# Kernel tuning notes

Measured on AMD Instinct MI355X. Metric: run time of the kernel, lower is better.

## Reference

```python
import jax, jax.numpy as jnp
import numpy as np

POLY_P = 3
POLY_N = 3
ACTIVATE = True
NUM_ATOMS = 100
BATCH = 100
N_TOTAL = NUM_ATOMS * BATCH          # 10000 nodes
N_EDGES = 1_000_000
F_COEF = 1.0
NCL = 3 * (POLY_P - 1) + 4 * (POLY_N - 1) + 8 + 4 + (12 if ACTIVATE else 0)  # 38
NFL = POLY_P + POLY_N + 3 + (3 if ACTIVATE else 0)                           # 12


def _safe_inv(v, eps=1e-2):
    # guard divide-by-near-zero in the negative-power library terms
    s = jnp.where(v >= 0, 1.0, -1.0)
    return 1.0 / jnp.where(jnp.abs(v) < eps, s * eps, v)


def coupled_fun_lib(x_i, x_j):
    # x_i, x_j: [E, 1] scalar node states gathered per edge
    d = x_j - x_i
    s = x_j + x_i
    feats = []
    for p in range(1, POLY_P):                      # 3*(P-1)
        feats += [x_i ** p, x_j ** p, d ** p]
    for n in range(1, POLY_N):                      # 4*(Q-1)
        feats += [_safe_inv(x_i) ** n, _safe_inv(x_j) ** n,
                  _safe_inv(d) ** n, _safe_inv(s) ** n]
    feats += [jnp.sin(d), jnp.cos(d), jnp.sin(s), jnp.cos(s),   # 8 trig
              jnp.sin(x_i), jnp.cos(x_i), jnp.sin(x_j), jnp.cos(x_j)]
    feats += [x_i * x_j, x_i * jnp.sin(x_j),                    # 4 cross terms
              x_j * jnp.sin(x_i), jnp.sin(d) * jnp.cos(s)]
    if ACTIVATE:                                    # 12 activation terms
        for v in (x_i, x_j, d, s):
            feats += [jnp.tanh(v), jax.nn.sigmoid(v), jax.nn.relu(v)]
    return jnp.concatenate(feats, axis=1)  # [E, NCL]


def fun_lib(x):
    # x: [N, 1]
    feats = [jnp.ones_like(x), jnp.sin(x), jnp.cos(x), x * jnp.sin(x)]
    for p in range(1, POLY_P):
        feats.append(x ** p)
    for n in range(1, POLY_N + 1):
        feats.append(_safe_inv(x) ** n)
    if ACTIVATE:
        feats += [jnp.tanh(x), jax.nn.sigmoid(x), jax.nn.relu(x)]
    return jnp.concatenate(feats, axis=1)  # [N, NFL]


def setup_inputs() -> dict:
    key = jax.random.key(0)
    k1, k2, k3 = jax.random.split(key, 3)
    x = jax.random.normal(k1, (N_TOTAL, 1), dtype=jnp.float32)
    edge_index = jax.random.randint(k2, (2, N_EDGES), 0, N_TOTAL, dtype=jnp.int32).astype(jnp.int64)
    c_mask = jnp.ones((NCL, 1), dtype=jnp.float32)
    f_mask = jnp.ones((NFL, 1), dtype=jnp.float32)
    wc_2 = jnp.concatenate([0.99 * jnp.ones((NCL, 1)), 0.01 * jnp.ones((NCL, 1))], 0).astype(jnp.float32)
    wf_2 = jnp.concatenate([0.99 * jnp.ones((NFL, 1)), 0.01 * jnp.ones((NFL, 1))], 0).astype(jnp.float32)
    edge_attr_all = jax.random.normal(k3, (NUM_ATOMS, NUM_ATOMS), dtype=jnp.float32)
    return {"t": 0, "x": x, "edge_index": edge_index, "c_mask": c_mask,
            "f_mask": f_mask, "wc_2": wc_2, "wf_2": wf_2,
            "edge_attr_all": edge_attr_all}


def reference(t, x, edge_index, c_mask, f_mask, wc_2, wf_2, edge_attr_all):
    src = edge_index[0]   # x_j (source)
    dst = edge_index[1]   # x_i (target / aggregation index)
    x_j = x[src]          # [E, 1]
    x_i = x[dst]          # [E, 1]

    # GSI_C: edge feature library (no_grad in torch -> stop_gradient)
    C_msg = jax.lax.stop_gradient(coupled_fun_lib(x_i, x_j))
    C_msg = jnp.concatenate([C_msg, -C_msg], axis=1)            # [E, 2*NCL]
    wc_1 = jnp.concatenate([c_mask, c_mask], axis=0)            # [2*NCL, 1]
    edge_attr = edge_attr_all[src % NUM_ATOMS, dst % NUM_ATOMS][:, None]  # [E, 1]
    msg = edge_attr * (C_msg @ (wc_1 * wc_2))                   # [E, 1]
    C = jax.ops.segment_sum(msg, dst, num_segments=N_TOTAL)     # 'add' aggr

    # GSI_F: node feature library
    F_msg = jax.lax.stop_gradient(fun_lib(x))
    F_msg = jnp.concatenate([F_msg, -F_msg], axis=1)            # [N, 2*NFL]
    wf_1 = jnp.concatenate([f_mask, f_mask], axis=0)
    F = F_msg @ (wf_1 * wf_2)                                   # [N, 1]

    return C + F_COEF * F
```

## Files before the change

kernel.cpp:

```cpp
#include <hip/hip_runtime.h>


#define NCL 38
#define NFL 12
#define NMAX 10240
#define EAN  10000
#define GRP 8

__device__ __forceinline__ float frcp(float v) { return __builtin_amdgcn_rcpf(v); }

__device__ __forceinline__ float safe_inv(float v) {
    float den = (fabsf(v) < 0.01f) ? ((v >= 0.0f) ? 0.01f : -0.01f) : v;
    return frcp(den);
}

__device__ __forceinline__ float edge_msg(float xi, float xj, const float* w) {
    float d = xj - xi;
    float s = xj + xi;
    float acc;
    acc  = w[0] * xi + w[1] * xj + w[2] * d;
    acc += w[3] * (xi * xi) + w[4] * (xj * xj) + w[5] * (d * d);
    float ii = safe_inv(xi), ij = safe_inv(xj), id = safe_inv(d), is = safe_inv(s);
    acc += w[6] * ii + w[7] * ij + w[8] * id + w[9] * is;
    acc += w[10] * (ii * ii) + w[11] * (ij * ij) + w[12] * (id * id) + w[13] * (is * is);
    float sd = __sinf(d), cd = __cosf(d);
    float ss = __sinf(s), cs = __cosf(s);
    float si = __sinf(xi), ci = __cosf(xi);
    float sj = __sinf(xj), cj = __cosf(xj);
    acc += w[14] * sd + w[15] * cd + w[16] * ss + w[17] * cs;
    acc += w[18] * si + w[19] * ci + w[20] * sj + w[21] * cj;
    acc += w[22] * (xi * xj) + w[23] * (xi * sj) + w[24] * (xj * si) + w[25] * (sd * cs);
    {
        float e = __expf(xi), e2 = e * e;
        acc += w[26] * ((e2 - 1.f) * frcp(e2 + 1.f)) + w[27] * (e * frcp(e + 1.f)) + w[28] * fmaxf(xi, 0.f);
    }
    {
        float e = __expf(xj), e2 = e * e;
        acc += w[29] * ((e2 - 1.f) * frcp(e2 + 1.f)) + w[30] * (e * frcp(e + 1.f)) + w[31] * fmaxf(xj, 0.f);
    }
    {
        float e = __expf(d), e2 = e * e;
        acc += w[32] * ((e2 - 1.f) * frcp(e2 + 1.f)) + w[33] * (e * frcp(e + 1.f)) + w[34] * fmaxf(d, 0.f);
    }
    {
        float e = __expf(s), e2 = e * e;
        acc += w[35] * ((e2 - 1.f) * frcp(e2 + 1.f)) + w[36] * (e * frcp(e + 1.f)) + w[37] * fmaxf(s, 0.f);
    }
    return acc;
}

__device__ __forceinline__ float node_F(float v, const float* wf) {
    float sv = __sinf(v), cv = __cosf(v);
    float iv = safe_inv(v);
    float e  = __expf(v), e2 = e * e;
    float th = (e2 - 1.f) * frcp(e2 + 1.f);
    float sg = e * frcp(e + 1.f);
    return wf[0] + wf[1] * sv + wf[2] * cv + wf[3] * (v * sv)
         + wf[4] * v + wf[5] * (v * v)
         + wf[6] * iv + wf[7] * (iv * iv) + wf[8] * (iv * iv * iv)
         + wf[9] * th + wf[10] * sg + wf[11] * fmaxf(v, 0.f);
}


__global__ void __launch_bounds__(1024) edge_lds_kernel(
        const float* __restrict__ x,
        const int* __restrict__ ei,
        const float* __restrict__ eattr,
        const float* __restrict__ c_mask,
        const float* __restrict__ wc2,
        float* __restrict__ scratch,
        int E, int N) {
    __shared__ float w[NCL];
    __shared__ float acc[NMAX];
    __shared__ float xs[NMAX];
    __shared__ float ea[EAN];
    if (threadIdx.x < NCL)
        w[threadIdx.x] = c_mask[threadIdx.x] * (wc2[threadIdx.x] - wc2[threadIdx.x + NCL]);
    {
        float4* a4 = (float4*)acc;
        for (int i = threadIdx.x; i < NMAX / 4; i += 1024) a4[i] = make_float4(0.f, 0.f, 0.f, 0.f);
        float4* x4 = (float4*)xs;
        int nx4 = N / 4;
        const float4* gx4 = (const float4*)x;
        for (int i = threadIdx.x; i < nx4; i += 1024) x4[i] = gx4[i];
        for (int i = 4 * nx4 + threadIdx.x; i < N; i += 1024) xs[i] = x[i];
        float4* e4 = (float4*)ea;
        const float4* ge4 = (const float4*)eattr;
        for (int i = threadIdx.x; i < EAN / 4; i += 1024) e4[i] = ge4[i];
    }
    __syncthreads();

    const int T = gridDim.x * 1024;
    const int t = blockIdx.x * 1024 + threadIdx.x;
    const int E4 = E & ~3;
    for (int e0 = 4 * t; e0 < E4; e0 += 4 * T) {
        int4 s4 = *(const int4*)(ei + e0);
        int4 d4 = *(const int4*)(ei + E + e0);
        int ss[4] = {s4.x, s4.y, s4.z, s4.w};
        int dd[4] = {d4.x, d4.y, d4.z, d4.w};
#pragma unroll
        for (int k = 0; k < 4; ++k) {
            int s = ss[k], d = dd[k];
            float m   = edge_msg(xs[d], xs[s], w);
            float eav = ea[(s % 100) * 100 + (d % 100)];
            atomicAdd(&acc[d], eav * m);
        }
    }
    if (t == 0) {
        for (int e = E4; e < E; ++e) {
            int s = ei[e], d = ei[E + e];
            float m   = edge_msg(xs[d], xs[s], w);
            float eav = ea[(s % 100) * 100 + (d % 100)];
            atomicAdd(&acc[d], eav * m);
        }
    }
    __syncthreads();
    float4* dst4 = (float4*)(scratch + (size_t)blockIdx.x * N);
    const float4* a4 = (const float4*)acc;
    int n4 = N / 4;
    for (int i = threadIdx.x; i < n4; i += 1024) dst4[i] = a4[i];
    for (int i = 4 * n4 + threadIdx.x; i < N; i += 1024)
        scratch[(size_t)blockIdx.x * N + i] = acc[i];
}

__global__ void __launch_bounds__(256) reduce1_kernel(
        const float* __restrict__ scratch, float* __restrict__ s2, int N, int B) {
    int n = blockIdx.x * 256 + threadIdx.x;
    if (n >= N) return;
    int per = B / GRP;
    const float* p = scratch + (size_t)(blockIdx.y * per) * N + n;
    float sum = 0.f;
    for (int b = 0; b < per; ++b) sum += p[(size_t)b * N];
    s2[(size_t)blockIdx.y * N + n] = sum;
}

__global__ void __launch_bounds__(256) reduce2_kernel(
        const float* __restrict__ x,
        const float* __restrict__ f_mask,
        const float* __restrict__ wf2,
        const float* __restrict__ s2,
        float* __restrict__ out, int N) {
    __shared__ float wf[NFL];
    if (threadIdx.x < NFL)
        wf[threadIdx.x] = f_mask[threadIdx.x] * (wf2[threadIdx.x] - wf2[threadIdx.x + NFL]);
    __syncthreads();
    int n = blockIdx.x * 256 + threadIdx.x;
    if (n >= N) return;
    float sum = node_F(x[n], wf);
#pragma unroll
    for (int g = 0; g < GRP; ++g) sum += s2[(size_t)g * N + n];
    out[n] = sum;
}


__global__ void __launch_bounds__(256) node_kernel(
        const float* __restrict__ x,
        const float* __restrict__ f_mask,
        const float* __restrict__ wf2,
        float* __restrict__ out, int n) {
    __shared__ float wf[NFL];
    if (threadIdx.x < NFL)
        wf[threadIdx.x] = f_mask[threadIdx.x] * (wf2[threadIdx.x] - wf2[threadIdx.x + NFL]);
    __syncthreads();
    int i = blockIdx.x * blockDim.x + threadIdx.x;
    if (i >= n) return;
    out[i] = node_F(x[i], wf);
}

__global__ void __launch_bounds__(256) edge_atomic_kernel(
        const float* __restrict__ x,
        const int* __restrict__ ei,
        const float* __restrict__ eattr,
        const float* __restrict__ c_mask,
        const float* __restrict__ wc2,
        float* __restrict__ out,
        int E) {
    __shared__ float w[NCL];
    if (threadIdx.x < NCL)
        w[threadIdx.x] = c_mask[threadIdx.x] * (wc2[threadIdx.x] - wc2[threadIdx.x + NCL]);
    __syncthreads();
    int t  = blockIdx.x * blockDim.x + threadIdx.x;
    int e0 = 4 * t;
    if (e0 + 3 < E) {
        int4 s4 = *(const int4*)(ei + e0);
        int4 d4 = *(const int4*)(ei + E + e0);
        int ss[4] = {s4.x, s4.y, s4.z, s4.w};
        int dd[4] = {d4.x, d4.y, d4.z, d4.w};
#pragma unroll
        for (int k = 0; k < 4; ++k) {
            int s = ss[k], d = dd[k];
            float m  = edge_msg(x[d], x[s], w);
            float ea = eattr[(s % 100) * 100 + (d % 100)];
            unsafeAtomicAdd(out + d, ea * m);
        }
    } else {
        for (int e = e0; e < E; ++e) {
            int s = ei[e], d = ei[E + e];
            float m  = edge_msg(x[d], x[s], w);
            float ea = eattr[(s % 100) * 100 + (d % 100)];
            unsafeAtomicAdd(out + d, ea * m);
        }
    }
}

extern "C" void kernel_launch(void* const* d_in, const int* in_sizes, int n_in,
                              void* d_out, int out_size, void* d_ws, size_t ws_size,
                              hipStream_t stream) {
    const float* x      = (const float*)d_in[1];
    const int*   ei     = (const int*)d_in[2];
    const float* c_mask = (const float*)d_in[3];
    const float* f_mask = (const float*)d_in[4];
    const float* wc2    = (const float*)d_in[5];
    const float* wf2    = (const float*)d_in[6];
    const float* eattr  = (const float*)d_in[7];
    float* out = (float*)d_out;

    int N = in_sizes[1];
    int E = in_sizes[2] / 2;

    int B = 0;
    if (N <= NMAX && in_sizes[7] == EAN) {
        const int tiers[3] = {256, 128, 64};
        for (int i = 0; i < 3; ++i) {
            size_t need = ((size_t)tiers[i] + GRP) * (size_t)N * 4;
            if (ws_size >= need) { B = tiers[i]; break; }
        }
    }

    if (B) {
        float* scratch = (float*)d_ws;
        float* s2      = scratch + (size_t)B * N;
        edge_lds_kernel<<<B, 1024, 0, stream>>>(x, ei, eattr, c_mask, wc2, scratch, E, N);
        dim3 g1((N + 255) / 256, GRP);
        reduce1_kernel<<<g1, 256, 0, stream>>>(scratch, s2, N, B);
        reduce2_kernel<<<(N + 255) / 256, 256, 0, stream>>>(x, f_mask, wf2, s2, out, N);
    } else {
        node_kernel<<<(N + 255) / 256, 256, 0, stream>>>(x, f_mask, wf2, out, N);
        int threads = (E + 3) / 4;
        edge_atomic_kernel<<<(threads + 255) / 256, 256, 0, stream>>>(x, ei, eattr, c_mask, wc2, out, E);
    }
}
```

Before: 96.11 us.

## Fuse edge, reduction and node stages into one cooperative kernel

Replaces the three-launch sequence (edge LDS accumulation, group reduce, final reduce plus node features) with a single cooperative kernel that uses grid-wide syncs between stages. This removes two kernel launch gaps and lets the final stage reuse x already held in LDS. In exchange it adds grid-sync overhead, and if the cooperative launch fails it falls back to the old three-kernel path.

```diff
diff --git a/kernel.cpp b/kernel.cpp
--- a/kernel.cpp
+++ b/kernel.cpp
@@ -1,4 +1,7 @@
 #include <hip/hip_runtime.h>
+#include <hip/hip_cooperative_groups.h>
+
+namespace cg = cooperative_groups;
 
 
 #define NCL 38
@@ -62,6 +65,102 @@
 }
 
 
+__global__ void __launch_bounds__(1024) fused_kernel(
+        const float* __restrict__ x,
+        const int* __restrict__ ei,
+        const float* __restrict__ eattr,
+        const float* __restrict__ c_mask,
+        const float* __restrict__ f_mask,
+        const float* __restrict__ wc2,
+        const float* __restrict__ wf2,
+        float* __restrict__ scratch,
+        float* __restrict__ s2,
+        float* __restrict__ out,
+        int E, int N, int B) {
+    __shared__ float w[NCL];
+    __shared__ float wf[NFL];
+    __shared__ float acc[NMAX];
+    __shared__ float xs[NMAX];
+    __shared__ float ea[EAN];
+
+    if (threadIdx.x < NCL)
+        w[threadIdx.x] = c_mask[threadIdx.x] * (wc2[threadIdx.x] - wc2[threadIdx.x + NCL]);
+    if (threadIdx.x >= 64 && threadIdx.x < 64 + NFL) {
+        int k = threadIdx.x - 64;
+        wf[k] = f_mask[k] * (wf2[k] - wf2[k + NFL]);
+    }
+    {
+        float4* a4 = (float4*)acc;
+        for (int i = threadIdx.x; i < NMAX / 4; i += 1024) a4[i] = make_float4(0.f, 0.f, 0.f, 0.f);
+        float4* x4 = (float4*)xs;
+        int nx4 = N / 4;
+        const float4* gx4 = (const float4*)x;
+        for (int i = threadIdx.x; i < nx4; i += 1024) x4[i] = gx4[i];
+        for (int i = 4 * nx4 + threadIdx.x; i < N; i += 1024) xs[i] = x[i];
+        float4* e4 = (float4*)ea;
+        const float4* ge4 = (const float4*)eattr;
+        for (int i = threadIdx.x; i < EAN / 4; i += 1024) e4[i] = ge4[i];
+    }
+    __syncthreads();
+
+    const int T = gridDim.x * 1024;
+    const int t = blockIdx.x * 1024 + threadIdx.x;
+
+    const int E4 = E & ~3;
+    for (int e0 = 4 * t; e0 < E4; e0 += 4 * T) {
+        int4 s4 = *(const int4*)(ei + e0);
+        int4 d4 = *(const int4*)(ei + E + e0);
+        int ss[4] = {s4.x, s4.y, s4.z, s4.w};
+        int dd[4] = {d4.x, d4.y, d4.z, d4.w};
+#pragma unroll
+        for (int k = 0; k < 4; ++k) {
+            int s = ss[k], d = dd[k];
+            float m   = edge_msg(xs[d], xs[s], w);
+            float eav = ea[(s % 100) * 100 + (d % 100)];
+            atomicAdd(&acc[d], eav * m);
+        }
+    }
+    if (t == 0) {
+        for (int e = E4; e < E; ++e) {
+            int s = ei[e], d = ei[E + e];
+            float m   = edge_msg(xs[d], xs[s], w);
+            float eav = ea[(s % 100) * 100 + (d % 100)];
+            atomicAdd(&acc[d], eav * m);
+        }
+    }
+    __syncthreads();
+    {
+        float4* dst4 = (float4*)(scratch + (size_t)blockIdx.x * N);
+        const float4* a4 = (const float4*)acc;
+        int n4 = N / 4;
+        for (int i = threadIdx.x; i < n4; i += 1024) dst4[i] = a4[i];
+        for (int i = 4 * n4 + threadIdx.x; i < N; i += 1024)
+            scratch[(size_t)blockIdx.x * N + i] = acc[i];
+    }
+    __threadfence();
+    cg::this_grid().sync();
+
+    const int per = B / GRP;
+    for (int u = t; u < GRP * N; u += T) {
+        int g = u / N, n = u - g * N;
+        const float* p = scratch + (size_t)(g * per) * N + n;
+        float sum = 0.f;
+#pragma unroll 8
+        for (int b = 0; b < per; ++b) sum += p[(size_t)b * N];
+        s2[(size_t)g * N + n] = sum;
+    }
+    __threadfence();
+    cg::this_grid().sync();
+
+    for (int n = t; n < N; n += T) {
+        float sum = node_F(xs[n], wf);
+#pragma unroll
+        for (int g = 0; g < GRP; ++g) sum += s2[(size_t)g * N + n];
+        out[n] = sum;
+    }
+}
+
+
 __global__ void __launch_bounds__(1024) edge_lds_kernel(
         const float* __restrict__ x,
         const int* __restrict__ ei,
@@ -89,7 +188,6 @@
         for (int i = threadIdx.x; i < EAN / 4; i += 1024) e4[i] = ge4[i];
     }
     __syncthreads();
-
     const int T = gridDim.x * 1024;
     const int t = blockIdx.x * 1024 + threadIdx.x;
     const int E4 = E & ~3;
@@ -230,10 +328,18 @@
     if (B) {
         float* scratch = (float*)d_ws;
         float* s2      = scratch + (size_t)B * N;
-        edge_lds_kernel<<<B, 1024, 0, stream>>>(x, ei, eattr, c_mask, wc2, scratch, E, N);
-        dim3 g1((N + 255) / 256, GRP);
-        reduce1_kernel<<<g1, 256, 0, stream>>>(scratch, s2, N, B);
-        reduce2_kernel<<<(N + 255) / 256, 256, 0, stream>>>(x, f_mask, wf2, s2, out, N);
+        void* args[] = {(void*)&x, (void*)&ei, (void*)&eattr, (void*)&c_mask,
+                        (void*)&f_mask, (void*)&wc2, (void*)&wf2,
+                        (void*)&scratch, (void*)&s2, (void*)&out,
+                        (void*)&E, (void*)&N, (void*)&B};
+        hipError_t err = hipLaunchCooperativeKernel((const void*)fused_kernel,
+                                                    dim3(B), dim3(1024), args, 0, stream);
+        if (err != hipSuccess) {
+            edge_lds_kernel<<<B, 1024, 0, stream>>>(x, ei, eattr, c_mask, wc2, scratch, E, N);
+            dim3 g1((N + 255) / 256, GRP);
+            reduce1_kernel<<<g1, 256, 0, stream>>>(scratch, s2, N, B);
+            reduce2_kernel<<<(N + 255) / 256, 256, 0, stream>>>(x, f_mask, wf2, s2, out, N);
+        }
     } else {
         node_kernel<<<(N + 255) / 256, 256, 0, stream>>>(x, f_mask, wf2, out, N);
         int threads = (E + 3) / 4;
```

Result: slower. 329.7 us (+243.0%).
